# Kernel tuning notes

Hardware: AMD Instinct MI355X
Metric: run time of the kernel (lower is better)

## Reference

```python
import jax, jax.numpy as jnp
import numpy as np

HEADS, DIM_HEAD, LANDMARKS, PINV_ITERS, CONV_K = 8, 64, 256, 6, 33


def iter_pinv(x, iters=PINV_ITERS):
    # Moore-Penrose iterative pseudo-inverse (lucidrains nystrom_attention)
    abs_x = jnp.abs(x)
    scale = abs_x.sum(-1).max() * abs_x.sum(-2).max()  # global maxes, as in torch.max
    z = jnp.swapaxes(x, -1, -2) / scale
    I = jnp.eye(x.shape[-1], dtype=x.dtype)
    for _ in range(iters):
        xz = x @ z
        z = 0.25 * z @ (13.0 * I - xz @ (15.0 * I - xz @ (7.0 * I - xz)))
    return z


def nystrom_attention(h, W_qkv, W_out, b_out, conv_w):
    b, n, _ = h.shape
    inner = HEADS * DIM_HEAD
    qkv = h @ W_qkv  # (b, n, 3*inner), bias=False
    q, k, v = jnp.split(qkv, 3, axis=-1)
    split_heads = lambda t: t.reshape(b, n, HEADS, DIM_HEAD).transpose(0, 2, 1, 3)
    q, k, v = split_heads(q), split_heads(k), split_heads(v)  # (b,h,n,dh)
    q = q * (DIM_HEAD ** -0.5)
    l = n // LANDMARKS  # tokens per landmark (n divisible by m, so no padding)
    q_l = q.reshape(b, HEADS, LANDMARKS, l, DIM_HEAD).mean(3)
    k_l = k.reshape(b, HEADS, LANDMARKS, l, DIM_HEAD).mean(3)
    sim1 = jnp.einsum('bhnd,bhmd->bhnm', q, k_l)      # (b,h,n,m)
    sim2 = jnp.einsum('bhmd,bhld->bhml', q_l, k_l)    # (b,h,m,m)
    sim3 = jnp.einsum('bhmd,bhnd->bhmn', q_l, k)      # (b,h,m,n)
    attn1 = jax.nn.softmax(sim1, -1)
    attn2 = jax.nn.softmax(sim2, -1)
    attn3 = jax.nn.softmax(sim3, -1)
    out = (attn1 @ iter_pinv(attn2)) @ (attn3 @ v)    # (b,h,n,dh)
    # residual depthwise conv along sequence dim: Conv2d(heads, heads, (33,1), groups=heads, no bias)
    res = jax.lax.conv_general_dilated(
        v, conv_w, window_strides=(1, 1),
        padding=((CONV_K // 2, CONV_K // 2), (0, 0)),
        feature_group_count=HEADS)
    out = out + res
    out = out.transpose(0, 2, 1, 3).reshape(b, n, inner)
    return out @ W_out + b_out


def setup_inputs() -> dict:
    key = jax.random.key(0)
    ks = jax.random.split(key, 8)
    N, Din, Dout = 8192, 1024, 256
    inner = HEADS * DIM_HEAD
    s = 0.02
    return {
        'x': jax.random.normal(ks[0], (1, N, Din), jnp.float32),
        'W_ft': jax.random.normal(ks[1], (Din, Dout), jnp.float32) * s,
        'b_ft': jnp.zeros((Dout,), jnp.float32),
        'W_qkv': jax.random.normal(ks[2], (Dout, 3 * inner), jnp.float32) * s,
        'W_out': jax.random.normal(ks[3], (inner, Dout), jnp.float32) * s,
        'b_out': jnp.zeros((Dout,), jnp.float32),
        'conv_w': jax.random.normal(ks[4], (HEADS, 1, CONV_K, 1), jnp.float32) * s,
        'W_score': jax.random.normal(ks[5], (Dout, 1), jnp.float32) * s,
        'b_score': jnp.zeros((1,), jnp.float32),
    }


def reference(x, W_ft, b_ft, W_qkv, W_out, b_out, conv_w, W_score, b_score):
    # feature_transform: Linear -> Dropout (identity in eval) -> ReLU
    h = jax.nn.relu(x @ W_ft + b_ft)                 # (1, N, Dout)
    af = nystrom_attention(h, W_qkv, W_out, b_out, conv_w)
    # score_layer: Linear -> Dropout -> ReLU
    scores = jax.nn.relu(af @ W_score + b_score)     # (1, N, 1)
    scores = scores[0].T                             # (1, N)
    weights = jax.nn.softmax(scores, axis=1)         # (1, N)
    aggregated = weights @ h[0]                      # (1, Dout)
    return aggregated, weights
```

## Files before the change

### kernel.cpp

```cpp
#include <hip/hip_runtime.h>

typedef unsigned short u16;
typedef __attribute__((ext_vector_type(8))) short s16x8;
typedef __attribute__((ext_vector_type(4))) float f32x4;
typedef __attribute__((ext_vector_type(8))) unsigned short u16x8;

__device__ inline float b2f(u16 u) {
  unsigned x = ((unsigned)u) << 16;
  return __builtin_bit_cast(float, x);
}
__device__ inline u16 f2b(float f) {
  unsigned u = __builtin_bit_cast(unsigned, f);
  u += 0x7fffu + ((u >> 16) & 1u);
  return (u16)(u >> 16);
}

#define GLL(src, dst) __builtin_amdgcn_global_load_lds( \
    (const __attribute__((address_space(1))) unsigned int*)(src), \
    (__attribute__((address_space(3))) unsigned int*)(dst), 16, 0, 0)

struct MP {
  const u16* A; const u16* B;
  u16* C; u16* Ct; float* Cf; u16* vTo;
  const u16* Aadd; const float* bias;
  const float* Ws; float* sc; const float* wconst;
  int M, N, K;
  int lda, ldb, ldc, ldct, ldcf, ldaadd;
  long long bA, bB, bC, bCt, bCf, bAadd;
  float alpha, beta;
  int relu, scale_cols; float colscale;
  int kchunks;
};

template<int BM, int BN, bool F32A>
__global__ __launch_bounds__(256) void gemm_mfma(MP p)
{
  constexpr int WM = BM / 2, WN = BN / 2;
  constexpr int FM = WM / 16, FN = WN / 16;
  constexpr int APAN = BM / 16, BPAN = BN / 16, NPAN = APAN + BPAN;
  constexpr int APW = (APAN + 3) / 4;
  __shared__ __align__(16) u16 lds[2 * NPAN * 512];

  const int tid = threadIdx.x, lane = tid & 63, wid = tid >> 6;
  const int bz = blockIdx.z;
  const int batch = (p.kchunks > 1) ? bz / p.kchunks : bz;
  const int kc    = (p.kchunks > 1) ? bz % p.kchunks : 0;
  const u16* A = p.A + (long long)batch * p.bA + (long long)kc * p.K;
  const float* Af32 = (const float*)p.A + (long long)batch * p.bA + (long long)kc * p.K;
  const u16* B = p.B + (long long)batch * p.bB + (long long)kc * p.K;
  const int m0 = blockIdx.y * BM, n0 = blockIdx.x * BN;
  const int srow = lane & 15, skoff = (lane >> 4) * 8;
  const int wm0 = (wid >> 1) * WM, wn0 = (wid & 1) * WN;

  f32x4 acc[FM][FN];
#pragma unroll
  for (int i = 0; i < FM; i++)
#pragma unroll
    for (int j = 0; j < FN; j++) acc[i][j] = (f32x4){0.f, 0.f, 0.f, 0.f};

  float4 areg[APW][2];

  auto stage_all = [&](int sb, int kt) {
#pragma unroll
    for (int pp = wid; pp < NPAN; pp += 4) {
      const u16* src = (pp < APAN)
        ? A + (size_t)(m0 + pp * 16 + srow) * p.lda + kt + skoff
        : B + (size_t)(n0 + (pp - APAN) * 16 + srow) * p.ldb + kt + skoff;
      GLL(src, &lds[sb * (NPAN * 512) + pp * 512]);
    }
  };
  auto stage_b = [&](int sb, int kt) {
#pragma unroll
    for (int pp = APAN + wid; pp < NPAN; pp += 4) {
      const u16* src = B + (size_t)(n0 + (pp - APAN) * 16 + srow) * p.ldb + kt + skoff;
      GLL(src, &lds[sb * (NPAN * 512) + pp * 512]);
    }
  };
  auto load_a = [&](int kt) {
#pragma unroll
    for (int ap = 0; ap < APW; ap++) {
      int pp = wid + ap * 4;
      const float* src = Af32 + (size_t)(m0 + pp * 16 + srow) * p.lda + kt + skoff;
      areg[ap][0] = ((const float4*)src)[0];
      areg[ap][1] = ((const float4*)src)[1];
    }
  };
  auto write_a = [&](int sb) {
#pragma unroll
    for (int ap = 0; ap < APW; ap++) {
      int pp = wid + ap * 4;
      u16 t[8];
      t[0] = f2b(areg[ap][0].x); t[1] = f2b(areg[ap][0].y);
      t[2] = f2b(areg[ap][0].z); t[3] = f2b(areg[ap][0].w);
      t[4] = f2b(areg[ap][1].x); t[5] = f2b(areg[ap][1].y);
      t[6] = f2b(areg[ap][1].z); t[7] = f2b(areg[ap][1].w);
      *(s16x8*)&lds[sb * (NPAN * 512) + pp * 512 + lane * 8] = *(const s16x8*)t;
    }
  };
  auto compute = [&](int sb) {
    const int bo = sb * (NPAN * 512);
    s16x8 afr[FM], bfr[FN];
#pragma unroll
    for (int i = 0; i < FM; i++)
      afr[i] = *(const s16x8*)&lds[bo + (wm0 / 16 + i) * 512 + lane * 8];
#pragma unroll
    for (int j = 0; j < FN; j++)
      bfr[j] = *(const s16x8*)&lds[bo + (APAN + wn0 / 16 + j) * 512 + lane * 8];
#pragma unroll
    for (int i = 0; i < FM; i++)
#pragma unroll
      for (int j = 0; j < FN; j++)
        acc[i][j] = __builtin_amdgcn_mfma_f32_16x16x32_bf16(afr[i], bfr[j], acc[i][j], 0, 0, 0);
  };

  const int nt = p.K / 32;
  int buf = 0;
  if constexpr (F32A) { load_a(0); stage_b(0, 0); write_a(0); }
  else                { stage_all(0, 0); }
  asm volatile("s_waitcnt vmcnt(0)" ::: "memory");
  __syncthreads();

  for (int t = 0; t < nt; ++t) {
    if constexpr (F32A) {
      if (t + 1 < nt) { load_a((t + 1) * 32); stage_b(buf ^ 1, (t + 1) * 32); }
      compute(buf);
      if (t + 1 < nt) write_a(buf ^ 1);
    } else {
      if (t + 1 < nt) stage_all(buf ^ 1, (t + 1) * 32);
      compute(buf);
    }
    asm volatile("s_waitcnt vmcnt(0)" ::: "memory");
    __syncthreads();
    buf ^= 1;
  }

  const int r0 = (lane >> 4) * 4, c0 = lane & 15;

  if (p.Ws) {
    float* sb = (float*)lds;
#pragma unroll
    for (int i = 0; i < FM; i++)
#pragma unroll
      for (int q = 0; q < 4; q++) {
        float s = 0.f;
#pragma unroll
        for (int j = 0; j < FN; j++)
          s += acc[i][j][q] * p.Ws[wn0 + j * 16 + c0];
        s += __shfl_xor(s, 1); s += __shfl_xor(s, 2);
        s += __shfl_xor(s, 4); s += __shfl_xor(s, 8);
        if ((lane & 15) == 0) sb[(wid & 1) * 64 + wm0 + i * 16 + r0 + q] = s;
      }
    __syncthreads();
    if (tid < 64) {
      float v = sb[tid] + sb[64 + tid] + p.wconst[0];
      p.sc[m0 + tid] = fmaxf(v, 0.f);
    }
    return;
  }

#pragma unroll
  for (int i = 0; i < FM; i++) {
#pragma unroll
    for (int j = 0; j < FN; j++) {
#pragma unroll
      for (int q = 0; q < 4; q++) {
        const int gr = m0 + wm0 + i * 16 + r0 + q;
        const int gc = n0 + wn0 + j * 16 + c0;
        float c = p.alpha * acc[i][j][q];
        if (p.Aadd) c += p.beta * b2f(p.Aadd[(long long)batch * p.bAadd + (size_t)gr * p.ldaadd + gc]);
        if (p.bias) c += p.bias[gc];
        if (gc < p.scale_cols) c *= p.colscale;
        if (p.relu) c = fmaxf(c, 0.f);
        if (p.Cf) p.Cf[(long long)bz * p.bCf + (size_t)gr * p.ldcf + gc] = c;
        u16 b = f2b(c);
        if (p.C)  p.C [(long long)batch * p.bC + (size_t)gr * p.ldc + gc] = b;
        if (p.Ct) p.Ct[(long long)batch * p.bCt + (size_t)gc * p.ldct + gr] = b;
        if (p.vTo && gc >= 1024) p.vTo[(size_t)(gc - 1024) * 8192 + gr] = b;
      }
    }
  }
}

struct AVF { const u16 *qkvb, *ql, *vT; float *Cf, *den; };

__global__ __launch_bounds__(256) void av_fused(AVF p)
{
  __shared__ __align__(16) u16 lds[20480];
  const int tid = threadIdx.x, lane = tid & 63, wid = tid >> 6;
  const int bz = blockIdx.z, head = bz >> 4, kc = bz & 15;
  const int m0 = blockIdx.y * 128;
  const int srow = lane & 15, skoff = (lane >> 4) * 8;
  const int r0 = (lane >> 4) * 4, c0 = lane & 15;
  const u16* Kb = p.qkvb + 512 + (size_t)(kc * 512) * 1536 + head * 64;
  const u16* Vb = p.vT + (size_t)head * 524288 + kc * 512;
  const u16* QL = p.ql + head * 16384 + (size_t)m0 * 64;

#pragma unroll
  for (int q = 0; q < 4; q++) {
    int pid = wid * 4 + q, pr = pid >> 1, kc2 = pid & 1;
    GLL(QL + (size_t)(pr * 16 + srow) * 64 + kc2 * 32 + skoff, &lds[pid * 512]);
  }
  auto stage_kv = [&](int sb, int t) {
    int kr = wid >> 1, kc2 = wid & 1;
    GLL(Kb + (size_t)(t * 32 + kr * 16 + srow) * 1536 + kc2 * 32 + skoff,
        &lds[8192 + sb * 2048 + wid * 512]);
    GLL(Vb + (size_t)(wid * 16 + srow) * 8192 + t * 32 + skoff,
        &lds[12288 + sb * 2048 + wid * 512]);
  };

  f32x4 acc[4][2];
#pragma unroll
  for (int i = 0; i < 4; i++)
#pragma unroll
    for (int j = 0; j < 2; j++) acc[i][j] = (f32x4){0.f, 0.f, 0.f, 0.f};
  float den[2][4];
#pragma unroll
  for (int i = 0; i < 2; i++)
#pragma unroll
    for (int q = 0; q < 4; q++) den[i][q] = 0.f;

  const int nt = 16;
  int buf = 0;
  stage_kv(0, 0);
  asm volatile("s_waitcnt vmcnt(0)" ::: "memory");
  __syncthreads();

  for (int t = 0; t < nt; ++t) {
    if (t + 1 < nt) stage_kv(buf ^ 1, t + 1);
    f32x4 s[2][2];
#pragma unroll
    for (int i = 0; i < 2; i++)
#pragma unroll
      for (int j = 0; j < 2; j++) s[i][j] = (f32x4){0.f, 0.f, 0.f, 0.f};
#pragma unroll
    for (int t2 = 0; t2 < 2; t2++) {
      s16x8 aq[2], bk[2];
#pragma unroll
      for (int i = 0; i < 2; i++)
        aq[i] = *(const s16x8*)&lds[((wid * 2 + i) * 2 + t2) * 512 + lane * 8];
#pragma unroll
      for (int j = 0; j < 2; j++)
        bk[j] = *(const s16x8*)&lds[8192 + buf * 2048 + (j * 2 + t2) * 512 + lane * 8];
#pragma unroll
      for (int i = 0; i < 2; i++)
#pragma unroll
        for (int j = 0; j < 2; j++)
          s[i][j] = __builtin_amdgcn_mfma_f32_16x16x32_bf16(aq[i], bk[j], s[i][j], 0, 0, 0);
    }
#pragma unroll
    for (int i = 0; i < 2; i++)
#pragma unroll
      for (int j = 0; j < 2; j++)
#pragma unroll
        for (int q = 0; q < 4; q++) {
          float e = expf(s[i][j][q]);
          den[i][q] += e;
          int kk = j * 16 + c0;
          lds[16384 + (wid * 2 + i) * 512 + (r0 + q) * 8 + (kk >> 3) * 128 + (kk & 7)] = f2b(e);
        }
    asm volatile("s_waitcnt vmcnt(0)" ::: "memory");
    __syncthreads();
    {
      s16x8 afr[4], bfr[2];
#pragma unroll
      for (int i = 0; i < 4; i++)
        afr[i] = *(const s16x8*)&lds[16384 + ((wid >> 1) * 4 + i) * 512 + lane * 8];
#pragma unroll
      for (int j = 0; j < 2; j++)
        bfr[j] = *(const s16x8*)&lds[12288 + buf * 2048 + ((wid & 1) * 2 + j) * 512 + lane * 8];
#pragma unroll
      for (int i = 0; i < 4; i++)
#pragma unroll
        for (int j = 0; j < 2; j++)
          acc[i][j] = __builtin_amdgcn_mfma_f32_16x16x32_bf16(afr[i], bfr[j], acc[i][j], 0, 0, 0);
    }
    __syncthreads();
    buf ^= 1;
  }

#pragma unroll
  for (int i = 0; i < 4; i++)
#pragma unroll
    for (int j = 0; j < 2; j++)
#pragma unroll
      for (int q = 0; q < 4; q++) {
        const int gr = m0 + (wid >> 1) * 64 + i * 16 + r0 + q;
        const int gc = (wid & 1) * 32 + j * 16 + c0;
        p.Cf[(size_t)bz * 16384 + (size_t)gr * 64 + gc] = acc[i][j][q];
      }
#pragma unroll
  for (int i = 0; i < 2; i++)
#pragma unroll
    for (int q = 0; q < 4; q++) {
      float v = den[i][q];
      v += __shfl_xor(v, 1); v += __shfl_xor(v, 2);
      v += __shfl_xor(v, 4); v += __shfl_xor(v, 8);
      if (c0 == 0)
        p.den[(size_t)bz * 256 + m0 + wid * 32 + i * 16 + r0 + q] = v;
    }
}

struct FA1 { const u16 *qkvb, *kl, *MmT; u16 *af; };

__global__ __launch_bounds__(256) void fused_attn1(FA1 p)
{
  __shared__ __align__(16) u16 lds[36864];
  __shared__ float mb[4][64];
  const int tid = threadIdx.x, lane = tid & 63, wid = tid >> 6;
  const int head = blockIdx.y, n0 = blockIdx.x * 64;
  const int srow = lane & 15, skoff = (lane >> 4) * 8;
  const int rbase = (lane >> 4) * 4;

  for (int pid = wid; pid < 72; pid += 4) {
    const u16* src;
    if (pid < 8) {
      int pr = pid >> 1, kc = pid & 1;
      src = p.qkvb + (size_t)(n0 + pr * 16 + srow) * 1536 + head * 64 + kc * 32 + skoff;
    } else if (pid < 40) {
      int j = pid - 8, pr = j >> 1, kc = j & 1;
      src = p.kl + head * 16384 + (size_t)(pr * 16 + srow) * 64 + kc * 32 + skoff;
    } else {
      int j = pid - 40, pr = j >> 3, kc = j & 7;
      src = p.MmT + head * 16384 + (size_t)(pr * 16 + srow) * 256 + kc * 32 + skoff;
    }
    GLL(src, &lds[pid * 512]);
  }
  asm volatile("s_waitcnt vmcnt(0)" ::: "memory");
  __syncthreads();

  const int wr = (wid >> 1) * 32, ch_ = wid & 1;
  f32x4 s[2][8];
#pragma unroll
  for (int i = 0; i < 2; i++)
#pragma unroll
    for (int j = 0; j < 8; j++) s[i][j] = (f32x4){0.f, 0.f, 0.f, 0.f};
#pragma unroll
  for (int t = 0; t < 2; t++) {
    s16x8 a[2], b[8];
#pragma unroll
    for (int i = 0; i < 2; i++)
      a[i] = *(const s16x8*)&lds[(((wid >> 1) * 2 + i) * 2 + t) * 512 + lane * 8];
#pragma unroll
    for (int j = 0; j < 8; j++)
      b[j] = *(const s16x8*)&lds[4096 + ((ch_ * 8 + j) * 2 + t) * 512 + lane * 8];
#pragma unroll
    for (int i = 0; i < 2; i++)
#pragma unroll
      for (int j = 0; j < 8; j++)
        s[i][j] = __builtin_amdgcn_mfma_f32_16x16x32_bf16(a[i], b[j], s[i][j], 0, 0, 0);
  }
#pragma unroll
  for (int i = 0; i < 2; i++)
#pragma unroll
    for (int q = 0; q < 4; q++) {
      float rm = -INFINITY;
#pragma unroll
      for (int j = 0; j < 8; j++) rm = fmaxf(rm, s[i][j][q]);
#pragma unroll
      for (int off = 1; off < 16; off <<= 1) rm = fmaxf(rm, __shfl_xor(rm, off));
      if ((lane & 15) == 0) mb[ch_][wr + i * 16 + rbase + q] = rm;
    }
  __syncthreads();
  float m_[2][4];
#pragma unroll
  for (int i = 0; i < 2; i++)
#pragma unroll
    for (int q = 0; q < 4; q++)
      m_[i][q] = fmaxf(mb[0][wr + i * 16 + rbase + q], mb[1][wr + i * 16 + rbase + q]);
#pragma unroll
  for (int i = 0; i < 2; i++)
#pragma unroll
    for (int q = 0; q < 4; q++) {
      float ss = 0.f;
#pragma unroll
      for (int j = 0; j < 8; j++) {
        float e = expf(s[i][j][q] - m_[i][q]);
        s[i][j][q] = e; ss += e;
      }
#pragma unroll
      for (int off = 1; off < 16; off <<= 1) ss += __shfl_xor(ss, off);
      if ((lane & 15) == 0) mb[2 + ch_][wr + i * 16 + rbase + q] = ss;
    }
  __syncthreads();
#pragma unroll
  for (int i = 0; i < 2; i++)
#pragma unroll
    for (int q = 0; q < 4; q++) {
      int row = wr + i * 16 + rbase + q;
      float inv = 1.f / (mb[2][row] + mb[3][row]);
#pragma unroll
      for (int j = 0; j < 8; j++)
        lds[(size_t)row * 264 + ch_ * 128 + j * 16 + (lane & 15)] = f2b(s[i][j][q] * inv);
    }
  __syncthreads();
  const int wr2 = (wid >> 1) * 32, wd2 = (wid & 1) * 32;
  f32x4 acc[2][2];
#pragma unroll
  for (int i = 0; i < 2; i++)
#pragma unroll
    for (int jd = 0; jd < 2; jd++) acc[i][jd] = (f32x4){0.f, 0.f, 0.f, 0.f};
#pragma unroll
  for (int t = 0; t < 8; t++) {
    s16x8 a[2], b[2];
#pragma unroll
    for (int i = 0; i < 2; i++)
      a[i] = *(const s16x8*)&lds[(size_t)(wr2 + i * 16 + (lane & 15)) * 264 + t * 32 + (lane >> 4) * 8];
#pragma unroll
    for (int jd = 0; jd < 2; jd++)
      b[jd] = *(const s16x8*)&lds[20480 + (((wid & 1) * 2 + jd) * 8 + t) * 512 + lane * 8];
#pragma unroll
    for (int i = 0; i < 2; i++)
#pragma unroll
      for (int jd = 0; jd < 2; jd++)
        acc[i][jd] = __builtin_amdgcn_mfma_f32_16x16x32_bf16(a[i], b[jd], acc[i][jd], 0, 0, 0);
  }
#pragma unroll
  for (int i = 0; i < 2; i++)
#pragma unroll
    for (int jd = 0; jd < 2; jd++)
#pragma unroll
      for (int q = 0; q < 4; q++)
        p.af[(size_t)(n0 + wr2 + i * 16 + rbase + q) * 512 + head * 64 + wd2 + jd * 16 + (lane & 15)]
            = f2b(acc[i][jd][q]);
}

__global__ void conv_res_add_bf16(const u16* __restrict__ qkvb,
                                  const float* __restrict__ convw,
                                  u16* __restrict__ af)
{
  __shared__ float vt[96][64];
  const int h = blockIdx.y, n0 = blockIdx.x * 64;
  const int t = threadIdx.x, ch = t & 63, r0 = t >> 6;
  for (int r = r0; r < 96; r += 4) {
    int n = n0 - 16 + r;
    float v = 0.f;
    if (n >= 0 && n < 8192) v = b2f(qkvb[(size_t)n * 1536 + 1024 + h * 64 + ch]);
    vt[r][ch] = v;
  }
  __syncthreads();
  float w[33];
#pragma unroll
  for (int j = 0; j < 33; j++) w[j] = convw[h * 33 + j];
  for (int tl = r0; tl < 64; tl += 4) {
    float acc = 0.f;
#pragma unroll
    for (int j = 0; j < 33; j++) acc += w[j] * vt[tl + j][ch];
    size_t o = (size_t)(n0 + tl) * 512 + h * 64 + ch;
    af[o] = f2b(b2f(af[o]) + acc);
  }
}

__global__ void fused_tail(const float* __restrict__ scores,
                           const u16* __restrict__ hb, float* __restrict__ out)
{
  __shared__ float red[256];
  const int t = threadIdx.x, c = blockIdx.x;
  float e[32];
  float m = -INFINITY;
#pragma unroll
  for (int i = 0; i < 32; i++) { e[i] = scores[t + i * 256]; m = fmaxf(m, e[i]); }
  red[t] = m; __syncthreads();
  for (int s = 128; s; s >>= 1) { if (t < s) red[t] = fmaxf(red[t], red[t + s]); __syncthreads(); }
  m = red[0]; __syncthreads();
  float ls = 0.f;
#pragma unroll
  for (int i = 0; i < 32; i++) { e[i] = expf(e[i] - m); ls += e[i]; }
  red[t] = ls; __syncthreads();
  for (int s = 128; s; s >>= 1) { if (t < s) red[t] += red[t + s]; __syncthreads(); }
  const float inv = 1.f / red[0];
  __syncthreads();

  if (c < 256) {
    float acc = 0.f;
#pragma unroll
    for (int i = 0; i < 32; i++)
      acc += e[i] * inv * b2f(hb[(size_t)(t + i * 256) * 256 + c]);
    red[t] = acc; __syncthreads();
    for (int s = 128; s; s >>= 1) { if (t < s) red[t] += red[t + s]; __syncthreads(); }
    if (t == 0) out[c] = red[0];
  } else {
#pragma unroll
    for (int i = 0; i < 32; i++) out[256 + t + i * 256] = e[i] * inv;
  }
}

__global__ void prescale(const u16* __restrict__ x2, float* __restrict__ sbuf)
{
  const int h = blockIdx.x, t = threadIdx.x;
  const u16* X = x2 + ((size_t)h << 16);
  float cs = 0.f;
  for (int r = 0; r < 256; r++) cs += fabsf(b2f(X[r * 256 + t]));
  float rs = 0.f;
  for (int c4 = 0; c4 < 256; c4 += 4) {
    ushort4 v = *(const ushort4*)(X + (size_t)t * 256 + c4);
    rs += fabsf(b2f(v.x)) + fabsf(b2f(v.y)) + fabsf(b2f(v.z)) + fabsf(b2f(v.w));
  }
  __shared__ float red[512];
  red[t] = rs; red[256 + t] = cs;
  __syncthreads();
  for (int s = 128; s; s >>= 1) {
    if (t < s) {
      red[t] = fmaxf(red[t], red[t + s]);
      red[256 + t] = fmaxf(red[256 + t], red[256 + t + s]);
    }
    __syncthreads();
  }
  if (t == 0) { sbuf[h] = red[0]; sbuf[8 + h] = red[256]; }
}

__global__ void pinv_init(const u16* __restrict__ x2, const float* __restrict__ sbuf,
                          u16* __restrict__ z0, u16* __restrict__ z0T)
{
  __shared__ u16 tile[64][80];
  const int t = threadIdx.x;
  const size_t base = (size_t)blockIdx.y << 16;
  const int tr = (blockIdx.x >> 2) * 64, tc = (blockIdx.x & 3) * 64;
  const u16* X = x2 + base;

  float mr = -INFINITY, mc = -INFINITY;
#pragma unroll
  for (int i = 0; i < 8; i++) {
    mr = fmaxf(mr, sbuf[i]);
    mc = fmaxf(mc, sbuf[8 + i]);
  }
  const float inv = 1.f / (mr * mc);

  {
    int r = t >> 2, cg = (t & 3) * 16;
#pragma unroll
    for (int v4 = 0; v4 < 4; v4++) {
      ushort4 v = *(const ushort4*)(X + (size_t)(tr + r) * 256 + tc + cg + v4 * 4);
      v.x = f2b(b2f(v.x) * inv); v.y = f2b(b2f(v.y) * inv);
      v.z = f2b(b2f(v.z) * inv); v.w = f2b(b2f(v.w) * inv);
      *(ushort4*)(z0T + base + (size_t)(tr + r) * 256 + tc + cg + v4 * 4) = v;
      *(ushort4*)&tile[r][cg + v4 * 4] = v;
    }
  }
  __syncthreads();
  {
    int c = t >> 2, rg = (t & 3) * 16;
    u16 o[16];
#pragma unroll
    for (int e = 0; e < 16; e++) o[e] = tile[rg + e][c];
#pragma unroll
    for (int v4 = 0; v4 < 4; v4++)
      *(ushort4*)(z0 + base + (size_t)(tc + c) * 256 + tr + rg + v4 * 4) = *(ushort4*)&o[v4 * 4];
  }
}

struct PG {
  const u16 *U, *V, *Xadd, *XaddT;
  u16 *DR, *DT;
  float alpha, beta;
};

template<bool WD, bool WDT>
__global__ __launch_bounds__(256) void pinv_gemm(PG p)
{
  __shared__ __align__(16) u16 lds[65536 / 2];
  const int tid = threadIdx.x, lane = tid & 63, wid = tid >> 6;
  const size_t base = (size_t)blockIdx.z << 16;
  const u16* U = p.U + base;
  const u16* V = p.V + base;
  const int m0 = blockIdx.y * 64, n0 = blockIdx.x * 64;
  const int srow = lane & 15, skoff = (lane >> 4) * 8;
  const int wr = (wid >> 1) * 32, wc = (wid & 1) * 32;

#pragma unroll
  for (int q = 0; q < 16; q++) {
    const int pid = wid * 16 + q;
    const int rg = (pid >> 3) & 3, t = pid & 7;
    const u16* src = (pid < 32)
      ? U + (size_t)(m0 + rg * 16 + srow) * 256 + t * 32 + skoff
      : V + (size_t)(n0 + rg * 16 + srow) * 256 + t * 32 + skoff;
    GLL(src, &lds[pid * 512]);
  }
  asm volatile("s_waitcnt vmcnt(0)" ::: "memory");
  __syncthreads();

  f32x4 acc[2][2], accT[2][2];
#pragma unroll
  for (int i = 0; i < 2; i++)
#pragma unroll
    for (int j = 0; j < 2; j++) {
      acc[i][j] = (f32x4){0.f, 0.f, 0.f, 0.f};
      accT[i][j] = (f32x4){0.f, 0.f, 0.f, 0.f};
    }

#pragma unroll
  for (int t = 0; t < 8; t++) {
    s16x8 afr[2], bfr[2];
#pragma unroll
    for (int i = 0; i < 2; i++)
      afr[i] = *(const s16x8*)&lds[((wr / 16 + i) * 8 + t) * 512 + lane * 8];
#pragma unroll
    for (int j = 0; j < 2; j++)
      bfr[j] = *(const s16x8*)&lds[(32 + (wc / 16 + j) * 8 + t) * 512 + lane * 8];
#pragma unroll
    for (int i = 0; i < 2; i++)
#pragma unroll
      for (int j = 0; j < 2; j++) {
        if constexpr (WD)
          acc[i][j] = __builtin_amdgcn_mfma_f32_16x16x32_bf16(afr[i], bfr[j], acc[i][j], 0, 0, 0);
        if constexpr (WDT)
          accT[j][i] = __builtin_amdgcn_mfma_f32_16x16x32_bf16(bfr[j], afr[i], accT[j][i], 0, 0, 0);
      }
  }

  const int r0 = (lane >> 4) * 4, c0 = lane & 15;
  if constexpr (WD) {
    const u16* Xa = p.Xadd ? p.Xadd + base : nullptr;
    u16* DR = p.DR + base;
#pragma unroll
    for (int i = 0; i < 2; i++)
#pragma unroll
      for (int j = 0; j < 2; j++)
#pragma unroll
        for (int q = 0; q < 4; q++) {
          const int gr = m0 + wr + i * 16 + r0 + q;
          const int gc = n0 + wc + j * 16 + c0;
          float v = p.alpha * acc[i][j][q];
          if (Xa) v += p.beta * b2f(Xa[(size_t)gr * 256 + gc]);
          DR[(size_t)gr * 256 + gc] = f2b(v);
        }
  }
  if constexpr (WDT) {
    const u16* Xt = p.XaddT ? p.XaddT + base : nullptr;
    u16* DT = p.DT + base;
#pragma unroll
    for (int j = 0; j < 2; j++)
#pragma unroll
      for (int i = 0; i < 2; i++)
#pragma unroll
        for (int q = 0; q < 4; q++) {
          const int gn = n0 + wc + j * 16 + r0 + q;
          const int gm = m0 + wr + i * 16 + c0;
          float v = p.alpha * accT[j][i][q];
          if (Xt) v += p.beta * b2f(Xt[(size_t)gn * 256 + gm]);
          DT[(size_t)gn * 256 + gm] = f2b(v);
        }
  }
}

struct PR1 { const u16 *A, *At, *z; u16 *B, *Bt, *G, *Gt, *W; };

__global__ __launch_bounds__(256) void pinv_r1(PR1 p)
{
  __shared__ __align__(16) u16 lds[32768];
  const int tid = threadIdx.x, lane = tid & 63, wid = tid >> 6;
  const int prob = blockIdx.z >> 3;
  const size_t base = (size_t)(blockIdx.z & 7) << 16;
  const u16* U = (prob ? p.z : p.A) + base;
  const u16* V = p.At + base;
  const int m0 = blockIdx.y * 64, n0 = blockIdx.x * 64;
  const int srow = lane & 15, skoff = (lane >> 4) * 8;
  const int wr = (wid >> 1) * 32, wc = (wid & 1) * 32;

#pragma unroll
  for (int q = 0; q < 16; q++) {
    const int pid = wid * 16 + q;
    const int rg = (pid >> 3) & 3, t = pid & 7;
    const u16* src = (pid < 32)
      ? U + (size_t)(m0 + rg * 16 + srow) * 256 + t * 32 + skoff
      : V + (size_t)(n0 + rg * 16 + srow) * 256 + t * 32 + skoff;
    GLL(src, &lds[pid * 512]);
  }
  asm volatile("s_waitcnt vmcnt(0)" ::: "memory");
  __syncthreads();

  f32x4 acc[2][2], accT[2][2];
#pragma unroll
  for (int i = 0; i < 2; i++)
#pragma unroll
    for (int j = 0; j < 2; j++) {
      acc[i][j] = (f32x4){0.f, 0.f, 0.f, 0.f};
      accT[i][j] = (f32x4){0.f, 0.f, 0.f, 0.f};
    }

#pragma unroll
  for (int t = 0; t < 8; t++) {
    s16x8 afr[2], bfr[2];
#pragma unroll
    for (int i = 0; i < 2; i++)
      afr[i] = *(const s16x8*)&lds[((wr / 16 + i) * 8 + t) * 512 + lane * 8];
#pragma unroll
    for (int j = 0; j < 2; j++)
      bfr[j] = *(const s16x8*)&lds[(32 + (wc / 16 + j) * 8 + t) * 512 + lane * 8];
#pragma unroll
    for (int i = 0; i < 2; i++)
#pragma unroll
      for (int j = 0; j < 2; j++) {
        acc[i][j] = __builtin_amdgcn_mfma_f32_16x16x32_bf16(afr[i], bfr[j], acc[i][j], 0, 0, 0);
        if (prob == 0)
          accT[j][i] = __builtin_amdgcn_mfma_f32_16x16x32_bf16(bfr[j], afr[i], accT[j][i], 0, 0, 0);
      }
  }

  const int r0 = (lane >> 4) * 4, c0 = lane & 15;
  if (prob == 0) {
    const u16* Ab  = p.A  + base;
    const u16* Atb = p.At + base;
    u16 *Bv = p.B + base, *Btv = p.Bt + base;
    u16 *Gv = p.G + base, *Gtv = p.Gt + base;
#pragma unroll
    for (int i = 0; i < 2; i++)
#pragma unroll
      for (int j = 0; j < 2; j++)
#pragma unroll
        for (int q = 0; q < 4; q++) {
          const int gr = m0 + wr + i * 16 + r0 + q;
          const int gc = n0 + wc + j * 16 + c0;
          float b = acc[i][j][q];
          float a = b2f(Ab[(size_t)gr * 256 + gc]);
          Bv[(size_t)gr * 256 + gc] = f2b(b);
          Gv[(size_t)gr * 256 + gc] = f2b(7.f * a - b);
        }
#pragma unroll
    for (int j = 0; j < 2; j++)
#pragma unroll
      for (int i = 0; i < 2; i++)
#pragma unroll
        for (int q = 0; q < 4; q++) {
          const int gn = n0 + wc + j * 16 + r0 + q;
          const int gm = m0 + wr + i * 16 + c0;
          float bt = accT[j][i][q];
          float at = b2f(Atb[(size_t)gn * 256 + gm]);
          Btv[(size_t)gn * 256 + gm] = f2b(bt);
          Gtv[(size_t)gn * 256 + gm] = f2b(7.f * at - bt);
        }
  } else {
    u16* Wv = p.W + base;
#pragma unroll
    for (int i = 0; i < 2; i++)
#pragma unroll
      for (int j = 0; j < 2; j++)
#pragma unroll
        for (int q = 0; q < 4; q++) {
          const int gr = m0 + wr + i * 16 + r0 + q;
          const int gc = n0 + wc + j * 16 + c0;
          Wv[(size_t)gr * 256 + gc] = f2b(acc[i][j][q]);
        }
  }
}

struct PR2 { const u16 *W, *G, *Gt, *B, *Bt, *z, *A, *At; u16 *zo, *Ao, *Aot; };

__global__ __launch_bounds__(256) void pinv_r2(PR2 p)
{
  __shared__ __align__(16) u16 lds[32768];
  const int tid = threadIdx.x, lane = tid & 63, wid = tid >> 6;
  const int prob = blockIdx.z >> 3;
  const size_t base = (size_t)(blockIdx.z & 7) << 16;
  const u16* U = (prob ? p.G  : p.W ) + base;
  const u16* V = (prob ? p.Bt : p.Gt) + base;
  const int m0 = blockIdx.y * 64, n0 = blockIdx.x * 64;
  const int srow = lane & 15, skoff = (lane >> 4) * 8;
  const int wr = (wid >> 1) * 32, wc = (wid & 1) * 32;

#pragma unroll
  for (int q = 0; q < 16; q++) {
    const int pid = wid * 16 + q;
    const int rg = (pid >> 3) & 3, t = pid & 7;
    const u16* src = (pid < 32)
      ? U + (size_t)(m0 + rg * 16 + srow) * 256 + t * 32 + skoff
      : V + (size_t)(n0 + rg * 16 + srow) * 256 + t * 32 + skoff;
    GLL(src, &lds[pid * 512]);
  }
  asm volatile("s_waitcnt vmcnt(0)" ::: "memory");
  __syncthreads();

  f32x4 acc[2][2], accT[2][2];
#pragma unroll
  for (int i = 0; i < 2; i++)
#pragma unroll
    for (int j = 0; j < 2; j++) {
      acc[i][j] = (f32x4){0.f, 0.f, 0.f, 0.f};
      accT[i][j] = (f32x4){0.f, 0.f, 0.f, 0.f};
    }

#pragma unroll
  for (int t = 0; t < 8; t++) {
    s16x8 afr[2], bfr[2];
#pragma unroll
    for (int i = 0; i < 2; i++)
      afr[i] = *(const s16x8*)&lds[((wr / 16 + i) * 8 + t) * 512 + lane * 8];
#pragma unroll
    for (int j = 0; j < 2; j++)
      bfr[j] = *(const s16x8*)&lds[(32 + (wc / 16 + j) * 8 + t) * 512 + lane * 8];
#pragma unroll
    for (int i = 0; i < 2; i++)
#pragma unroll
      for (int j = 0; j < 2; j++) {
        acc[i][j] = __builtin_amdgcn_mfma_f32_16x16x32_bf16(afr[i], bfr[j], acc[i][j], 0, 0, 0);
        if (prob)
          accT[j][i] = __builtin_amdgcn_mfma_f32_16x16x32_bf16(bfr[j], afr[i], accT[j][i], 0, 0, 0);
      }
  }

  const int r0 = (lane >> 4) * 4, c0 = lane & 15;
  if (prob == 0) {
    const u16* Zb = p.z + base;
    const u16* Wb = p.W + base;
    u16* Zo = p.zo + base;
#pragma unroll
    for (int i = 0; i < 2; i++)
#pragma unroll
      for (int j = 0; j < 2; j++)
#pragma unroll
        for (int q = 0; q < 4; q++) {
          const int gr = m0 + wr + i * 16 + r0 + q;
          const int gc = n0 + wc + j * 16 + c0;
          float v = 0.25f * acc[i][j][q]
                  + 3.25f * b2f(Zb[(size_t)gr * 256 + gc])
                  - 3.75f * b2f(Wb[(size_t)gr * 256 + gc]);
          Zo[(size_t)gr * 256 + gc] = f2b(v);
        }
  } else {
    const u16* Ab  = p.A  + base;
    const u16* Bb  = p.B  + base;
    const u16* Atb = p.At + base;
    const u16* Btb = p.Bt + base;
    u16* Ao  = p.Ao  + base;
    u16* Aot = p.Aot + base;
#pragma unroll
    for (int i = 0; i < 2; i++)
#pragma unroll
      for (int j = 0; j < 2; j++)
#pragma unroll
        for (int q = 0; q < 4; q++) {
          const int gr = m0 + wr + i * 16 + r0 + q;
          const int gc = n0 + wc + j * 16 + c0;
          float v = 0.25f * acc[i][j][q]
                  + 3.25f * b2f(Ab[(size_t)gr * 256 + gc])
                  - 3.75f * b2f(Bb[(size_t)gr * 256 + gc]);
          Ao[(size_t)gr * 256 + gc] = f2b(v);
        }
#pragma unroll
    for (int j = 0; j < 2; j++)
#pragma unroll
      for (int i = 0; i < 2; i++)
#pragma unroll
        for (int q = 0; q < 4; q++) {
          const int gn = n0 + wc + j * 16 + r0 + q;
          const int gm = m0 + wr + i * 16 + c0;
          float v = 0.25f * accT[j][i][q]
                  + 3.25f * b2f(Atb[(size_t)gn * 256 + gm])
                  - 3.75f * b2f(Btb[(size_t)gn * 256 + gm]);
          Aot[(size_t)gn * 256 + gm] = f2b(v);
        }
  }
}

__global__ void prep_weights(const float* __restrict__ Wft, const float* __restrict__ Wqkv,
                             const float* __restrict__ Wout, u16* __restrict__ WftT,
                             u16* __restrict__ WqkvT, u16* __restrict__ WoutT,
                             const float* __restrict__ bout, const float* __restrict__ Wsc,
                             const float* __restrict__ bsc, float* __restrict__ wconst)
{
  int idx = blockIdx.x * 256 + threadIdx.x;
  if (blockIdx.x == 0 && threadIdx.x < 64) {
    int c = threadIdx.x * 4;
    float s = bout[c] * Wsc[c] + bout[c + 1] * Wsc[c + 1]
            + bout[c + 2] * Wsc[c + 2] + bout[c + 3] * Wsc[c + 3];
    for (int off = 1; off < 64; off <<= 1) s += __shfl_xor(s, off);
    if (threadIdx.x == 0) wconst[0] = s + bsc[0];
  }
  if (idx < 262144) {
    int r = idx & 1023, c = idx >> 10;
    WftT[idx] = f2b(Wft[(size_t)r * 256 + c]);
  } else if (idx < 655360) {
    int i = idx - 262144;
    int r = i & 255, c = i >> 8;
    WqkvT[i] = f2b(Wqkv[(size_t)r * 1536 + c]);
  } else {
    int i = idx - 655360;
    int r = i & 511, c = i >> 9;
    WoutT[i] = f2b(Wout[(size_t)r * 256 + c]);
  }
}

__global__ void landmark_means(const u16* __restrict__ qkvb,
                               u16* __restrict__ ql, u16* __restrict__ kl)
{
  int idx = blockIdx.x * 256 + threadIdx.x;
  int which = idx >> 17, r = idx & 131071;
  int h = r >> 14, m = (r >> 6) & 255, d = r & 63;
  const u16* src = qkvb + (which ? 512 : 0) + h * 64 + d;
  float s = 0.f; int n0 = m * 32;
  for (int i = 0; i < 32; i++) s += b2f(src[(size_t)(n0 + i) * 1536]);
  (which ? kl : ql)[r] = f2b(s * (1.f / 32.f));
}

__global__ void softmax_rows_bf16_256(u16* __restrict__ d)
{
  const int row = blockIdx.x * 4 + (threadIdx.x >> 6);
  const int lane = threadIdx.x & 63;
  ushort4* p = (ushort4*)(d + (size_t)row * 256);
  ushort4 raw = p[lane];
  float v0 = b2f(raw.x), v1 = b2f(raw.y), v2 = b2f(raw.z), v3 = b2f(raw.w);
  float mx = fmaxf(fmaxf(v0, v1), fmaxf(v2, v3));
  for (int off = 1; off < 64; off <<= 1) mx = fmaxf(mx, __shfl_xor(mx, off));
  v0 = expf(v0 - mx); v1 = expf(v1 - mx); v2 = expf(v2 - mx); v3 = expf(v3 - mx);
  float s = v0 + v1 + v2 + v3;
  for (int off = 1; off < 64; off <<= 1) s += __shfl_xor(s, off);
  float inv = 1.f / s;
  raw.x = f2b(v0 * inv); raw.y = f2b(v1 * inv); raw.z = f2b(v2 * inv); raw.w = f2b(v3 * inv);
  p[lane] = raw;
}

__global__ void reduce_avT(const float* __restrict__ avp, const float* __restrict__ den,
                           u16* __restrict__ avT)
{
  int idx = blockIdx.x * 256 + threadIdx.x;
  int m = idx & 255, d = (idx >> 8) & 63, h = idx >> 14;
  float s = 0.f, l = 0.f;
  for (int c = 0; c < 16; c++) {
    s += avp[((size_t)(h * 16 + c)) * 16384 + m * 64 + d];
    l += den[(size_t)(h * 16 + c) * 256 + m];
  }
  avT[((size_t)h * 64 + d) * 256 + m] = f2b(s / l);
}

extern "C" void kernel_launch(void* const* d_in, const int* in_sizes, int n_in,
                              void* d_out, int out_size, void* d_ws, size_t ws_size,
                              hipStream_t stream)
{
  const float* x       = (const float*)d_in[0];
  const float* W_ft    = (const float*)d_in[1];
  const float* b_ft    = (const float*)d_in[2];
  const float* W_qkv   = (const float*)d_in[3];
  const float* W_out   = (const float*)d_in[4];
  const float* b_out   = (const float*)d_in[5];
  const float* conv_w  = (const float*)d_in[6];
  const float* W_score = (const float*)d_in[7];
  const float* b_score = (const float*)d_in[8];
  float* out = (float*)d_out;

  char* W = (char*)d_ws;
  auto alloc = [&](size_t bytes) { char* r = W; W += (bytes + 255) & ~(size_t)255; return r; };
  u16* WftT  = (u16*)alloc(256ull * 1024 * 2);
  u16* WqkvT = (u16*)alloc(1536ull * 256 * 2);
  u16* WoutT = (u16*)alloc(256ull * 512 * 2);
  u16* hb    = (u16*)alloc(8192ull * 256 * 2);
  u16* qkvb  = (u16*)alloc(8192ull * 1536 * 2);
  u16* ql    = (u16*)alloc(8ull * 256 * 64 * 2);
  u16* kl    = (u16*)alloc(8ull * 256 * 64 * 2);
  u16* x2    = (u16*)alloc(8ull * 256 * 256 * 2);
  u16* z0    = (u16*)alloc(8ull * 256 * 256 * 2);
  u16* z0T   = (u16*)alloc(8ull * 256 * 256 * 2);
  u16* zp    = (u16*)alloc(8ull * 256 * 256 * 2);
  u16* Amat  = (u16*)alloc(8ull * 256 * 256 * 2);
  u16* AmatT = (u16*)alloc(8ull * 256 * 256 * 2);
  u16* Am2   = (u16*)alloc(8ull * 256 * 256 * 2);
  u16* Am2T  = (u16*)alloc(8ull * 256 * 256 * 2);
  u16* Bm    = (u16*)alloc(8ull * 256 * 256 * 2);
  u16* BmT   = (u16*)alloc(8ull * 256 * 256 * 2);
  u16* Gm    = (u16*)alloc(8ull * 256 * 256 * 2);
  u16* GmT   = (u16*)alloc(8ull * 256 * 256 * 2);
  u16* Wm    = (u16*)alloc(8ull * 256 * 256 * 2);
  u16* vT    = (u16*)alloc(8ull * 64 * 8192 * 2);
  float* avp = (float*)alloc(8ull * 16 * 256 * 64 * 4);
  float* denp = (float*)alloc(128ull * 256 * 4);
  u16* avT   = (u16*)alloc(8ull * 64 * 256 * 2);
  u16* MmT   = (u16*)alloc(8ull * 64 * 256 * 2);
  u16* af    = (u16*)alloc(8192ull * 512 * 2);
  float* sbuf   = (float*)alloc(256);
  float* scores = (float*)alloc(8192 * 4);
  float* wconst = (float*)alloc(256);

  auto mp = [](const u16* A, const u16* B, int M, int N, int K,
               int lda, int ldb, long long bA, long long bB) {
    MP p{}; p.A = A; p.B = B; p.M = M; p.N = N; p.K = K;
    p.lda = lda; p.ldb = ldb; p.bA = bA; p.bB = bB;
    p.alpha = 1.f; p.beta = 0.f; p.kchunks = 1; return p;
  };

  prep_weights<<<3072, 256, 0, stream>>>(W_ft, W_qkv, W_out, WftT, WqkvT, WoutT,
                                         b_out, W_score, b_score, wconst);

  { MP p = mp((const u16*)x, WftT, 8192, 256, 1024, 1024, 1024, 0, 0);
    p.C = hb; p.ldc = 256; p.bias = b_ft; p.relu = 1;
    gemm_mfma<64, 256, true><<<dim3(1, 128, 1), 256, 0, stream>>>(p); }

  { MP p = mp(hb, WqkvT, 8192, 1536, 256, 256, 256, 0, 0);
    p.C = qkvb; p.ldc = 1536; p.scale_cols = 512; p.colscale = 0.125f; p.vTo = vT;
    gemm_mfma<128, 128, false><<<dim3(12, 64, 1), 256, 0, stream>>>(p); }

  landmark_means<<<1024, 256, 0, stream>>>(qkvb, ql, kl);

  { MP p = mp(ql, kl, 256, 256, 64, 64, 64, 16384, 16384);
    p.C = x2; p.ldc = 256; p.bC = 65536;
    gemm_mfma<64, 64, false><<<dim3(4, 4, 8), 256, 0, stream>>>(p); }
  softmax_rows_bf16_256<<<512, 256, 0, stream>>>(x2);

  prescale<<<8, 256, 0, stream>>>(x2, sbuf);
  pinv_init<<<dim3(16, 8), 256, 0, stream>>>(x2, sbuf, z0, z0T);
  { PG p{x2, z0T, nullptr, nullptr, Amat, AmatT, 1.f, 0.f};
    pinv_gemm<true, true><<<dim3(4, 4, 8), 256, 0, stream>>>(p); }
  {
    const dim3 b(256);
    u16 *zr = z0, *zo = zp;
    u16 *Ar = Amat, *Art = AmatT, *Ao = Am2, *Aot = Am2T;
    for (int it = 0; it < 6; it++) {
      { PR1 r{Ar, Art, zr, Bm, BmT, Gm, GmT, Wm};
        pinv_r1<<<dim3(4, 4, 16), b, 0, stream>>>(r); }
      { PR2 r{Wm, Gm, GmT, Bm, BmT, zr, Ar, Art, zo, Ao, Aot};
        pinv_r2<<<dim3(4, 4, (it == 5) ? 8 : 16), b, 0, stream>>>(r); }
      u16* t;
      t = zr; zr = zo; zo = t;
      t = Ar; Ar = Ao; Ao = t;
      t = Art; Art = Aot; Aot = t;
    }
  }

  { AVF p{qkvb, ql, vT, avp, denp};
    av_fused<<<dim3(1, 2, 128), 256, 0, stream>>>(p); }
  reduce_avT<<<512, 256, 0, stream>>>(avp, denp, avT);

  { MP p = mp(z0, avT, 256, 64, 256, 256, 256, 65536, 16384);
    p.Ct = MmT; p.ldct = 256; p.bCt = 16384;
    gemm_mfma<64, 64, false><<<dim3(1, 4, 8), 256, 0, stream>>>(p); }

  { FA1 fp{qkvb, kl, MmT, af};
    fused_attn1<<<dim3(128, 8), 256, 0, stream>>>(fp); }

  conv_res_add_bf16<<<dim3(128, 8), 256, 0, stream>>>(qkvb, conv_w, af);

  { MP p = mp(af, WoutT, 8192, 256, 512, 512, 512, 0, 0);
    p.Ws = W_score; p.sc = scores; p.wconst = wconst;
    gemm_mfma<64, 256, false><<<dim3(1, 128, 1), 256, 0, stream>>>(p); }

  fused_tail<<<257, 256, 0, stream>>>(scores, hb, out);
}
```

Measured before the change: 357.9 us.

## Split-K the feature-transform and output GEMMs into four partials with reductions

The first GEMM (8192x256x1024) and the output/score GEMM now run with four K chunks over a 4x larger grid, since 128 blocks underfill the GPU. The first GEMM writes fp32 partials that a new kernel sums, adds bias, applies ReLU and converts to bf16. The score GEMM writes four partial score vectors that the tail kernel sums with the bias constant before the softmax. In exchange it adds an extra kernel launch and fp32 partial traffic of about 32 MB.

```diff
diff --git a/kernel.cpp b/kernel.cpp
--- a/kernel.cpp
+++ b/kernel.cpp
@@ -23,7 +23,7 @@
   const u16* A; const u16* B;
   u16* C; u16* Ct; float* Cf; u16* vTo;
   const u16* Aadd; const float* bias;
-  const float* Ws; float* sc; const float* wconst;
+  const float* Ws; float* sc;
   int M, N, K;
   int lda, ldb, ldc, ldct, ldcf, ldaadd;
   long long bA, bB, bC, bCt, bCf, bAadd;
@@ -151,10 +151,8 @@
         if ((lane & 15) == 0) sb[(wid & 1) * 64 + wm0 + i * 16 + r0 + q] = s;
       }
     __syncthreads();
-    if (tid < 64) {
-      float v = sb[tid] + sb[64 + tid] + p.wconst[0];
-      p.sc[m0 + tid] = fmaxf(v, 0.f);
-    }
+    if (tid < 64)
+      p.sc[(size_t)bz * 8192 + m0 + tid] = sb[tid] + sb[64 + tid];
     return;
   }
 
@@ -181,6 +179,24 @@
   }
 }
 
+__global__ void reduce_bias_bf16(const float* __restrict__ parts,
+                                 const float* __restrict__ bias,
+                                 u16* __restrict__ out)
+{
+  const int i4 = blockIdx.x * 256 + threadIdx.x;
+  float4 s = ((const float4*)parts)[i4];
+#pragma unroll
+  for (int k = 1; k < 4; k++) {
+    float4 v = ((const float4*)parts)[(size_t)k * 524288 + i4];
+    s.x += v.x; s.y += v.y; s.z += v.z; s.w += v.w;
+  }
+  const float4 b = ((const float4*)bias)[i4 & 63];
+  s.x = fmaxf(s.x + b.x, 0.f); s.y = fmaxf(s.y + b.y, 0.f);
+  s.z = fmaxf(s.z + b.z, 0.f); s.w = fmaxf(s.w + b.w, 0.f);
+  ushort4 o; o.x = f2b(s.x); o.y = f2b(s.y); o.z = f2b(s.z); o.w = f2b(s.w);
+  ((ushort4*)out)[i4] = o;
+}
+
 struct AVF { const u16 *qkvb, *ql, *vT; float *Cf, *den; };
 
 __global__ __launch_bounds__(256) void av_fused(AVF p)
@@ -450,15 +466,22 @@
   }
 }
 
-__global__ void fused_tail(const float* __restrict__ scores,
+__global__ void fused_tail(const float* __restrict__ sp,
+                           const float* __restrict__ wconst,
                            const u16* __restrict__ hb, float* __restrict__ out)
 {
   __shared__ float red[256];
   const int t = threadIdx.x, c = blockIdx.x;
+  const float wc = wconst[0];
   float e[32];
   float m = -INFINITY;
 #pragma unroll
-  for (int i = 0; i < 32; i++) { e[i] = scores[t + i * 256]; m = fmaxf(m, e[i]); }
+  for (int i = 0; i < 32; i++) {
+    int idx = t + i * 256;
+    float v = sp[idx] + sp[8192 + idx] + sp[16384 + idx] + sp[24576 + idx] + wc;
+    v = fmaxf(v, 0.f);
+    e[i] = v; m = fmaxf(m, v);
+  }
   red[t] = m; __syncthreads();
   for (int s = 128; s; s >>= 1) { if (t < s) red[t] = fmaxf(red[t], red[t + s]); __syncthreads(); }
   m = red[0]; __syncthreads();
@@ -964,8 +987,9 @@
   u16* avT   = (u16*)alloc(8ull * 64 * 256 * 2);
   u16* MmT   = (u16*)alloc(8ull * 64 * 256 * 2);
   u16* af    = (u16*)alloc(8192ull * 512 * 2);
+  float* gpart = (float*)alloc(4ull * 8192 * 256 * 4);
   float* sbuf   = (float*)alloc(256);
-  float* scores = (float*)alloc(8192 * 4);
+  float* scores = (float*)alloc(4ull * 8192 * 4);
   float* wconst = (float*)alloc(256);
 
   auto mp = [](const u16* A, const u16* B, int M, int N, int K,
@@ -978,9 +1002,10 @@
   prep_weights<<<3072, 256, 0, stream>>>(W_ft, W_qkv, W_out, WftT, WqkvT, WoutT,
                                          b_out, W_score, b_score, wconst);
 
-  { MP p = mp((const u16*)x, WftT, 8192, 256, 1024, 1024, 1024, 0, 0);
-    p.C = hb; p.ldc = 256; p.bias = b_ft; p.relu = 1;
-    gemm_mfma<64, 256, true><<<dim3(1, 128, 1), 256, 0, stream>>>(p); }
+  { MP p = mp((const u16*)x, WftT, 8192, 256, 256, 1024, 1024, 0, 0);
+    p.kchunks = 4; p.Cf = gpart; p.ldcf = 256; p.bCf = 2097152;
+    gemm_mfma<64, 256, true><<<dim3(1, 128, 4), 256, 0, stream>>>(p); }
+  reduce_bias_bf16<<<2048, 256, 0, stream>>>(gpart, b_ft, hb);
 
   { MP p = mp(hb, WqkvT, 8192, 1536, 256, 256, 256, 0, 0);
     p.C = qkvb; p.ldc = 1536; p.scale_cols = 512; p.colscale = 0.125f; p.vTo = vT;
@@ -1026,9 +1051,9 @@
 
   conv_res_add_bf16<<<dim3(128, 8), 256, 0, stream>>>(qkvb, conv_w, af);
 
-  { MP p = mp(af, WoutT, 8192, 256, 512, 512, 512, 0, 0);
-    p.Ws = W_score; p.sc = scores; p.wconst = wconst;
-    gemm_mfma<64, 256, false><<<dim3(1, 128, 1), 256, 0, stream>>>(p); }
-
-  fused_tail<<<257, 256, 0, stream>>>(scores, hb, out);
-}
+  { MP p = mp(af, WoutT, 8192, 256, 128, 512, 512, 0, 0);
+    p.kchunks = 4; p.Ws = W_score; p.sc = scores;
+    gemm_mfma<64, 256, false><<<dim3(1, 128, 4), 256, 0, stream>>>(p); }
+
+  fused_tail<<<257, 256, 0, stream>>>(scores, wconst, hb, out);
+}
```

Result: faster. 331.3 us (-7.4%).
